# Kernel optimization log

Measured on AMD Instinct MI355X. Metric: run time of the kernel, lower is better.

The kernel has to match this reference:

```python
import jax, jax.numpy as jnp
import numpy as np
import math

DIM = 512
HEADS = 8
DIM_HEAD = 64
SCALE = math.sqrt(DIM_HEAD)
EPS = 1e-12


def rms_norm(x, g):
    # F.normalize(x, dim=1) * g * sqrt(dim); x: [B, C, H, W], g: [C]
    inv = jax.lax.rsqrt(jnp.sum(x * x, axis=1, keepdims=True) + EPS)
    return x * inv * g[None, :, None, None] * jnp.asarray(math.sqrt(x.shape[1]), x.dtype)


def setup_inputs() -> dict:
    key = jax.random.key(0)
    k1, k2, k3 = jax.random.split(key, 3)
    B, H, W = 8, 64, 64
    hidden = HEADS * DIM_HEAD
    x = jax.random.normal(k1, (B, DIM, H, W), dtype=jnp.float32)
    w_qkv = jax.random.normal(k2, (3 * hidden, DIM), dtype=jnp.float32) * (1.0 / math.sqrt(DIM))
    w_out = jax.random.normal(k3, (DIM, hidden), dtype=jnp.float32) * (1.0 / math.sqrt(hidden))
    b_out = jnp.zeros((DIM,), dtype=jnp.float32)
    g1 = jnp.ones((DIM,), dtype=jnp.float32)
    g2 = jnp.ones((DIM,), dtype=jnp.float32)
    return {"x": x, "g1": g1, "w_qkv": w_qkv, "w_out": w_out, "b_out": b_out, "g2": g2}


def reference(x, g1, w_qkv, w_out, b_out, g2):
    B, C, H, W = x.shape
    n = H * W
    xn = rms_norm(x, g1)
    # 1x1 conv == channel matmul: [B, 3*hidden, H, W]
    qkv = jnp.einsum('bchw,oc->bohw', xn, w_qkv)
    q, k, v = jnp.split(qkv, 3, axis=1)
    # b (h c) x y -> b h c n
    def to_heads(t):
        return t.reshape(B, HEADS, DIM_HEAD, n)
    q, k, v = to_heads(q), to_heads(k), to_heads(v)
    q = jax.nn.softmax(q, axis=2) / SCALE   # softmax over channel dim d
    k = jax.nn.softmax(k, axis=3)           # softmax over spatial dim n
    context = jnp.einsum('bhdn,bhen->bhde', k, v)   # [B, H, d, e]
    out = jnp.einsum('bhde,bhdn->bhen', context, q) # [B, H, e, n]
    out = out.reshape(B, HEADS * DIM_HEAD, H, W)
    out = jnp.einsum('bchw,oc->bohw', out, w_out) + b_out[None, :, None, None]
    return rms_norm(out, g2)
```

## Files before the change

kernel.cpp:

```cpp
#include <hip/hip_runtime.h>


typedef unsigned short u16;
typedef __attribute__((ext_vector_type(8))) short short8;
typedef __attribute__((ext_vector_type(4))) short short4_t;
typedef __attribute__((ext_vector_type(4))) float f32x4;

static constexpr size_t XN_B = (size_t)512 * 4096;
static constexpr size_t KV_B = (size_t)1024 * 4096;
static constexpr float SQRT512 = 22.62741699796952f;

typedef const __attribute__((address_space(1))) unsigned int gu32;
typedef __attribute__((address_space(3))) unsigned int lu32;

__device__ __forceinline__ float b2f(u16 u){
  union { unsigned u; float f; } x; x.u = ((unsigned)u) << 16; return x.f;
}
__device__ __forceinline__ u16 f2b(float f){
  union { float f; unsigned u; } x; x.f = f;
  unsigned r = x.u + 0x7FFFu + ((x.u >> 16) & 1u);
  return (u16)(r >> 16);
}
__device__ __forceinline__ void gl16(const u16* g, u16* l){
  __builtin_amdgcn_global_load_lds((gu32*)g, (lu32*)l, 16, 0, 0);
}

__global__ __launch_bounds__(256)
void kprep(const float* __restrict__ wqkv, const float* __restrict__ wout,
           const float* __restrict__ g1, u16* __restrict__ dq, u16* __restrict__ dw,
           const float* __restrict__ x, u16* __restrict__ xnT){
  __shared__ u16 lt[32][514];
  __shared__ float red[256];
  __shared__ float invs[32];
  int bid = blockIdx.x;
  int t = threadIdx.x;
  if (bid < 1024){
    size_t i = ((size_t)bid * 256 + t) * 4;
    short4_t o;
    if (i < (size_t)786432){
      f32x4 v = *(const f32x4*)(wqkv + i);
      int c = (int)(i & 511);
      #pragma unroll
      for (int j = 0; j < 4; j++) o[j] = (short)f2b(v[j] * g1[c + j] * SQRT512);
      *(short4_t*)(dq + i) = o;
    } else {
      size_t off = i - 786432;
      f32x4 v = *(const f32x4*)(wout + off);
      #pragma unroll
      for (int j = 0; j < 4; j++) o[j] = (short)f2b(v[j]);
      *(short4_t*)(dw + off) = o;
    }
    return;
  }
  int pg0 = (bid - 1024) * 32;
  int b = pg0 >> 12, p0 = pg0 & 4095;
  int px = t & 31, chunk = t >> 5;
  const float* xp = x + (size_t)b * XN_B + p0 + px;
  float s = 0.f;
  #pragma unroll 4
  for (int c = chunk * 64; c < chunk * 64 + 64; ++c){
    float v = xp[(size_t)c * 4096];
    lt[px][c] = f2b(v);
    s += v * v;
  }
  red[t] = s;
  __syncthreads();
  if (chunk == 0){
    float tt = red[px] + red[px + 32] + red[px + 64] + red[px + 96]
             + red[px + 128] + red[px + 160] + red[px + 192] + red[px + 224];
    invs[px] = rsqrtf(tt + 1e-12f);
  }
  __syncthreads();
  int px2 = t >> 3, c0 = (t & 7) * 8;
  float iv = invs[px2];
  u16* dst = xnT + (size_t)(pg0 + px2) * 512;
  #pragma unroll
  for (int j = 0; j < 8; j++){
    int c = c0 + j * 64;
    short8 o;
    #pragma unroll
    for (int e = 0; e < 8; e++) o[e] = (short)f2b(b2f(lt[px2][c + e]) * iv);
    *(short8*)(dst + c) = o;
  }
}

template<int ADD_BIAS, int SMAX>
__global__ __launch_bounds__(512)
void gemm_big(const u16* __restrict__ Ab, long astr, int lda,
              const u16* __restrict__ Bb, long bstr, int ldb,
              u16* __restrict__ Cb, long cstr, int ldc,
              const float* __restrict__ bias)
{
  constexpr int NT = 16;
  const u16* A  = Ab + (size_t)blockIdx.z * astr;
  const u16* BT = Bb + (size_t)blockIdx.z * bstr;
  u16* C = Cb + (size_t)blockIdx.z * cstr;
  const int m0 = blockIdx.y * 256, n0 = blockIdx.x * 256;
  __shared__ u16 As[2][256 * 32];
  __shared__ u16 Bs[2][256 * 32];
  const int tid = threadIdx.x;
  const int lane = tid & 63, wid = tid >> 6;
  const int wr = (wid >> 2) * 128, wc = (wid & 3) * 64;
  const int fr = lane & 15, fq = lane >> 4;
  const int srow = tid >> 2;
  const int sslot = tid & 3;
  f32x4 acc[8][4] = {};

  auto STAGE = [&](int s, int t){
    const int k0 = t * 32;
    #pragma unroll
    for (int r = 0; r < 2; r++){
      int row = r * 128 + srow;
      int gj = (sslot ^ ((row >> 1) & 3)) * 8;
      gl16(A  + (size_t)(m0 + row) * lda + k0 + gj, &As[s][0] + r * 4096 + tid * 8);
      gl16(BT + (size_t)(n0 + row) * ldb + k0 + gj, &Bs[s][0] + r * 4096 + tid * 8);
    }
  };

  STAGE(0, 0);
  int cur = 0;
  for (int t = 0; t < NT; t++){
    if (t + 1 < NT){
      STAGE(cur ^ 1, t + 1);
      asm volatile("s_waitcnt vmcnt(4)" ::: "memory");
    } else {
      asm volatile("s_waitcnt vmcnt(0)" ::: "memory");
    }
    __builtin_amdgcn_s_barrier();
    __builtin_amdgcn_sched_barrier(0);
    short8 a[8], b[4];
    #pragma unroll
    for (int i = 0; i < 8; i++){
      int ra = wr + i * 16 + fr;
      a[i] = *(const short8*)(&As[cur][0] + ra * 32 + ((fq ^ ((ra >> 1) & 3)) * 8));
    }
    #pragma unroll
    for (int j = 0; j < 4; j++){
      int rb = wc + j * 16 + fr;
      b[j] = *(const short8*)(&Bs[cur][0] + rb * 32 + ((fq ^ ((rb >> 1) & 3)) * 8));
    }
    __builtin_amdgcn_s_setprio(1);
    #pragma unroll
    for (int i = 0; i < 8; i++)
      #pragma unroll
      for (int j = 0; j < 4; j++)
        acc[i][j] = __builtin_amdgcn_mfma_f32_16x16x32_bf16(a[i], b[j], acc[i][j], 0, 0, 0);
    __builtin_amdgcn_s_setprio(0);
    __builtin_amdgcn_sched_barrier(0);
    __builtin_amdgcn_s_barrier();
    cur ^= 1;
  }

  if constexpr (SMAX){
    #pragma unroll
    for (int i = 0; i < 8; i++)
      #pragma unroll
      for (int e = 0; e < 4; e++){
        float mx = fmaxf(fmaxf(acc[i][0][e], acc[i][1][e]),
                         fmaxf(acc[i][2][e], acc[i][3][e]));
        mx = fmaxf(mx, __shfl_xor(mx, 1));
        mx = fmaxf(mx, __shfl_xor(mx, 2));
        mx = fmaxf(mx, __shfl_xor(mx, 4));
        mx = fmaxf(mx, __shfl_xor(mx, 8));
        float p0 = __expf(acc[i][0][e] - mx);
        float p1 = __expf(acc[i][1][e] - mx);
        float p2 = __expf(acc[i][2][e] - mx);
        float p3 = __expf(acc[i][3][e] - mx);
        float s = p0 + p1 + p2 + p3;
        s += __shfl_xor(s, 1);
        s += __shfl_xor(s, 2);
        s += __shfl_xor(s, 4);
        s += __shfl_xor(s, 8);
        float r = 1.f / (s * 8.0f);
        acc[i][0][e] = p0 * r; acc[i][1][e] = p1 * r;
        acc[i][2][e] = p2 * r; acc[i][3][e] = p3 * r;
      }
  }
  #pragma unroll
  for (int i = 0; i < 8; i++)
    #pragma unroll
    for (int j = 0; j < 4; j++)
      #pragma unroll
      for (int e = 0; e < 4; e++){
        int row = m0 + wr + i * 16 + fq * 4 + e;
        int col = n0 + wc + j * 16 + fr;
        float v = acc[i][j][e];
        if constexpr (ADD_BIAS) v += bias[col];
        C[(size_t)row * ldc + col] = f2b(v);
      }
}

__global__ __launch_bounds__(256)
void gemm_kv(const u16* __restrict__ Wkv, const u16* __restrict__ xnT,
             u16* __restrict__ kvb, float* __restrict__ stats)
{
  constexpr int NT = 8;
  const int z = blockIdx.z;
  const u16* A  = Wkv;
  const u16* BT = xnT + (size_t)z * XN_B;
  u16* C = kvb + (size_t)z * KV_B;
  const int m0 = blockIdx.y * 128, n0 = blockIdx.x * 128;
  __shared__ u16 As[2][128 * 64];
  __shared__ u16 Bs[2][128 * 64];
  const int tid = threadIdx.x;
  const int srow0 = tid >> 3;
  const int schunk = tid & 7;
  const int lane = tid & 63, wid = tid >> 6;
  const int wr = (wid >> 1) * 64, wc = (wid & 1) * 64;
  const int fr = lane & 15, fq = lane >> 4;
  f32x4 acc[4][4] = {};

  auto STAGE = [&](int s, int t){
    const int k0 = t * 64;
    #pragma unroll
    for (int r = 0; r < 4; r++){
      int row = r * 32 + srow0;
      int gj = (schunk ^ (row & 7)) * 8;
      gl16(A  + (size_t)(m0 + row) * 512 + k0 + gj, &As[s][0] + r * 2048 + tid * 8);
      gl16(BT + (size_t)(n0 + row) * 512 + k0 + gj, &Bs[s][0] + r * 2048 + tid * 8);
    }
  };

  STAGE(0, 0);
  int cur = 0;
  for (int t = 0; t < NT; t++){
    if (t + 1 < NT){
      STAGE(cur ^ 1, t + 1);
      asm volatile("s_waitcnt vmcnt(8)" ::: "memory");
    } else {
      asm volatile("s_waitcnt vmcnt(0)" ::: "memory");
    }
    __builtin_amdgcn_s_barrier();
    __builtin_amdgcn_sched_barrier(0);
    #pragma unroll
    for (int ks = 0; ks < 2; ks++){
      short8 a[4], b[4];
      #pragma unroll
      for (int i = 0; i < 4; i++){
        int ra = wr + i * 16 + fr;
        a[i] = *(const short8*)(&As[cur][0] + ra * 64 + ((ks * 4 + fq) ^ (ra & 7)) * 8);
        int rb = wc + i * 16 + fr;
        b[i] = *(const short8*)(&Bs[cur][0] + rb * 64 + ((ks * 4 + fq) ^ (rb & 7)) * 8);
      }
      __builtin_amdgcn_s_setprio(1);
      #pragma unroll
      for (int i = 0; i < 4; i++)
        #pragma unroll
        for (int j = 0; j < 4; j++)
          acc[i][j] = __builtin_amdgcn_mfma_f32_16x16x32_bf16(a[i], b[j], acc[i][j], 0, 0, 0);
      __builtin_amdgcn_s_setprio(0);
    }
    __builtin_amdgcn_sched_barrier(0);
    __builtin_amdgcn_s_barrier();
    cur ^= 1;
  }

  const bool krows = (m0 < 512);
  #pragma unroll
  for (int i = 0; i < 4; i++)
    #pragma unroll
    for (int e = 0; e < 4; e++){
      int row = m0 + wr + i * 16 + fq * 4 + e;
      float s = 0.f;
      #pragma unroll
      for (int j = 0; j < 4; j++){
        int col = n0 + wc + j * 16 + fr;
        u16 vc = f2b(acc[i][j][e]);
        C[(size_t)row * 4096 + col] = vc;
        if (krows) s += __expf(b2f(vc));
      }
      if (krows){
        s += __shfl_xor(s, 1);
        s += __shfl_xor(s, 2);
        s += __shfl_xor(s, 4);
        s += __shfl_xor(s, 8);
        if (fr == 0) atomicAdd(stats + z * 512 + row, s);
      }
    }
}

__global__ __launch_bounds__(256)
void gemm_ctx(const u16* __restrict__ kv, float* __restrict__ P,
              const float* __restrict__ stats)
{
  constexpr int K = 1024;
  const int z = blockIdx.z;
  const int tid = threadIdx.x;
  const int ar = tid >> 2, ac = (tid & 3) * 8;
  int bh = z >> 2, sp = z & 3, b = bh >> 3, h = bh & 7;
  const u16* A  = kv + (size_t)b * KV_B + (size_t)(h * 64) * 4096 + sp * 1024;
  const u16* BT = kv + (size_t)b * KV_B + (size_t)(512 + h * 64) * 4096 + sp * 1024;
  float rsr = 1.f / stats[b * 512 + h * 64 + ar];
  __shared__ u16 As[64 * 40];
  __shared__ u16 Bs[64 * 40];
  const int wid = tid >> 6, lane = tid & 63;
  const int wr = (wid >> 1) * 32, wc = (wid & 1) * 32;
  const int lr = lane & 15, kb = lane >> 4;
  f32x4 acc[2][2] = {};
  for (int k0 = 0; k0 < K; k0 += 32){
    short8 av = *(const short8*)(A + (size_t)ar * 4096 + k0 + ac);
    short8 ao;
    #pragma unroll
    for (int e = 0; e < 8; e++)
      ao[e] = (short)f2b(__expf(b2f((u16)av[e])) * rsr);
    *(short8*)(As + ar * 40 + ac) = ao;
    *(short8*)(Bs + ar * 40 + ac) = *(const short8*)(BT + (size_t)ar * 4096 + k0 + ac);
    __syncthreads();
    short8 a0 = *(const short8*)(As + (wr +      lr) * 40 + kb * 8);
    short8 a1 = *(const short8*)(As + (wr + 16 + lr) * 40 + kb * 8);
    short8 b0 = *(const short8*)(Bs + (wc +      lr) * 40 + kb * 8);
    short8 b1 = *(const short8*)(Bs + (wc + 16 + lr) * 40 + kb * 8);
    acc[0][0] = __builtin_amdgcn_mfma_f32_16x16x32_bf16(a0, b0, acc[0][0], 0, 0, 0);
    acc[0][1] = __builtin_amdgcn_mfma_f32_16x16x32_bf16(a0, b1, acc[0][1], 0, 0, 0);
    acc[1][0] = __builtin_amdgcn_mfma_f32_16x16x32_bf16(a1, b0, acc[1][0], 0, 0, 0);
    acc[1][1] = __builtin_amdgcn_mfma_f32_16x16x32_bf16(a1, b1, acc[1][1], 0, 0, 0);
    __syncthreads();
  }
  #pragma unroll
  for (int mi = 0; mi < 2; mi++)
    #pragma unroll
    for (int ni = 0; ni < 2; ni++)
      #pragma unroll
      for (int j = 0; j < 4; j++){
        int row = wr + mi * 16 + kb * 4 + j;
        int col = wc + ni * 16 + lr;
        P[(size_t)z * 4096 + (size_t)row * 64 + col] = acc[mi][ni][j];
      }
}

__global__ __launch_bounds__(256)
void kctxw(const float* __restrict__ P, const u16* __restrict__ woutbf,
           u16* __restrict__ M)
{
  const int z = blockIdx.z;
  const int b = z >> 3, h = z & 7;
  const int m0 = blockIdx.y * 64;
  const int tid = threadIdx.x;
  __shared__ u16 As[64 * 72];
  __shared__ u16 Bs[64 * 72];
  {
    int r = tid >> 2, c0 = (tid & 3) * 16;
    const u16* wsrc = woutbf + (size_t)(m0 + r) * 512 + h * 64 + c0;
    *(short8*)(As + r * 72 + c0)     = *(const short8*)(wsrc);
    *(short8*)(As + r * 72 + c0 + 8) = *(const short8*)(wsrc + 8);
    const float* p = P + (size_t)z * 16384 + (size_t)r * 64 + c0;
    #pragma unroll
    for (int e = 0; e < 16; e++){
      float s = p[e] + p[e + 4096] + p[e + 8192] + p[e + 12288];
      Bs[r * 72 + c0 + e] = f2b(s);
    }
  }
  __syncthreads();
  const int wid = tid >> 6, lane = tid & 63;
  const int wr = (wid >> 1) * 32, wc = (wid & 1) * 32;
  const int lr = lane & 15, kb = lane >> 4;
  f32x4 acc[2][2] = {};
  #pragma unroll
  for (int k0 = 0; k0 < 64; k0 += 32){
    short8 a0 = *(const short8*)(As + (wr +      lr) * 72 + k0 + kb * 8);
    short8 a1 = *(const short8*)(As + (wr + 16 + lr) * 72 + k0 + kb * 8);
    short8 b0 = *(const short8*)(Bs + (wc +      lr) * 72 + k0 + kb * 8);
    short8 b1 = *(const short8*)(Bs + (wc + 16 + lr) * 72 + k0 + kb * 8);
    acc[0][0] = __builtin_amdgcn_mfma_f32_16x16x32_bf16(a0, b0, acc[0][0], 0, 0, 0);
    acc[0][1] = __builtin_amdgcn_mfma_f32_16x16x32_bf16(a0, b1, acc[0][1], 0, 0, 0);
    acc[1][0] = __builtin_amdgcn_mfma_f32_16x16x32_bf16(a1, b0, acc[1][0], 0, 0, 0);
    acc[1][1] = __builtin_amdgcn_mfma_f32_16x16x32_bf16(a1, b1, acc[1][1], 0, 0, 0);
  }
  #pragma unroll
  for (int mi = 0; mi < 2; mi++)
    #pragma unroll
    for (int ni = 0; ni < 2; ni++)
      #pragma unroll
      for (int j = 0; j < 4; j++){
        int row = m0 + wr + mi * 16 + kb * 4 + j;
        int col = wc + ni * 16 + lr;
        M[(size_t)b * 262144 + (size_t)row * 512 + h * 64 + col] = f2b(acc[mi][ni][j]);
      }
}

__global__ __launch_bounds__(256)
void krms2(const u16* __restrict__ o2, const float* __restrict__ g,
           float* __restrict__ out){
  __shared__ u16 lt[32][514];
  __shared__ float invs[32];
  __shared__ float gl[512];
  int t = threadIdx.x;
  int pg0 = blockIdx.x * 32;
  int b = pg0 >> 12, p0 = pg0 & 4095;
  gl[t] = g[t] * SQRT512;
  gl[t + 256] = g[t + 256] * SQRT512;
  int px2 = t >> 3, c0 = (t & 7) * 8;
  const u16* src = o2 + (size_t)(pg0 + px2) * 512;
  float s = 0.f;
  #pragma unroll
  for (int j = 0; j < 8; j++){
    int c = c0 + j * 64;
    short8 v = *(const short8*)(src + c);
    *(short8*)&lt[px2][c] = v;
    #pragma unroll
    for (int e = 0; e < 8; e++){ float f = b2f((u16)v[e]); s += f * f; }
  }
  s += __shfl_xor(s, 1); s += __shfl_xor(s, 2); s += __shfl_xor(s, 4);
  if ((t & 7) == 0) invs[px2] = rsqrtf(s + 1e-12f);
  __syncthreads();
  int c2 = t >> 2, pxc = (t & 3) * 8;
  float ivv[8];
  #pragma unroll
  for (int e = 0; e < 8; e++) ivv[e] = invs[pxc + e];
  #pragma unroll
  for (int pass = 0; pass < 8; pass++){
    int c = c2 + pass * 64;
    float gf = gl[c];
    float* dst = out + ((size_t)(b * 512 + c)) * 4096 + p0 + pxc;
    #pragma unroll
    for (int q = 0; q < 2; q++){
      f32x4 o;
      #pragma unroll
      for (int e = 0; e < 4; e++){
        int pp = q * 4 + e;
        o[e] = b2f(lt[pxc + pp][c]) * ivv[pp] * gf;
      }
      *(f32x4*)(dst + q * 4) = o;
    }
  }
}

extern "C" void kernel_launch(void* const* d_in, const int* in_sizes, int n_in,
                              void* d_out, int out_size, void* d_ws, size_t ws_size,
                              hipStream_t stream)
{
  (void)in_sizes; (void)n_in; (void)out_size; (void)ws_size;
  const float* x    = (const float*)d_in[0];
  const float* g1   = (const float*)d_in[1];
  const float* wqkv = (const float*)d_in[2];
  const float* wout = (const float*)d_in[3];
  const float* bout = (const float*)d_in[4];
  const float* g2   = (const float*)d_in[5];
  float* out = (float*)d_out;
  char* ws = (char*)d_ws;

  u16*   xnT   = (u16*)(ws);
  float* P     = (float*)(ws);
  u16*   M     = (u16*)(ws + (size_t)8388608);
  u16*   qT    = (u16*)(ws + (size_t)33554432);
  u16*   kv    = (u16*)(ws + (size_t)67108864);
  u16*   out2T = (u16*)(ws + (size_t)67108864);
  u16*   wbf   = (u16*)(ws + (size_t)134217728);
  u16*   wkvbf = wbf + (size_t)512 * 512;
  u16*   woutbf= (u16*)(ws + (size_t)135790592);
  float* stats = (float*)(ws + (size_t)136314880);

  hipMemsetAsync(stats, 0, 4096 * sizeof(float), stream);
  kprep<<<2048, 256, 0, stream>>>(wqkv, wout, g1, wbf, woutbf, x, xnT);
  gemm_big<0, 1><<<dim3(2, 128, 1), 512, 0, stream>>>(xnT, 0, 512, wbf, 0, 512,
                                                      qT, 0, 512, nullptr);
  gemm_kv<<<dim3(32, 8, 8), 256, 0, stream>>>(wkvbf, xnT, kv, stats);
  gemm_ctx<<<dim3(1, 1, 256), 256, 0, stream>>>(kv, P, stats);
  kctxw<<<dim3(1, 8, 64), 256, 0, stream>>>(P, woutbf, M);
  gemm_big<1, 0><<<dim3(2, 16, 8), 512, 0, stream>>>(qT, (long)4096 * 512, 512,
                                                     M, (long)262144, 512,
                                                     out2T, (long)4096 * 512, 512, bout);
  krms2<<<1024, 256, 0, stream>>>(out2T, g2, out);
}
```

Before: 198.8 us.

## Move softmax row-sum stats to separate kernel and double ctx split-K

Removes the exp-sum and atomicAdd epilogue from the KV GEMM and computes the reciprocal row sums in a dedicated kstats kernel that rereads the K rows. The context GEMM now splits the spatial dimension 8 ways instead of 4, launching 512 blocks, and kctxw reduces 8 partials. It also drops the setprio hints and the stats memset. The intent is to shorten the GEMM epilogue, avoid contended atomics, and fill more CUs in the context step. The cost is an extra launch, an extra pass over the K half of kv, and a larger partial buffer to reduce.

```diff
diff --git a/kernel.cpp b/kernel.cpp
--- a/kernel.cpp
+++ b/kernel.cpp
@@ -192,7 +192,7 @@
 
 __global__ __launch_bounds__(256)
 void gemm_kv(const u16* __restrict__ Wkv, const u16* __restrict__ xnT,
-             u16* __restrict__ kvb, float* __restrict__ stats)
+             u16* __restrict__ kvb)
 {
   constexpr int NT = 8;
   const int z = blockIdx.z;
@@ -242,55 +242,63 @@
         int rb = wc + i * 16 + fr;
         b[i] = *(const short8*)(&Bs[cur][0] + rb * 64 + ((ks * 4 + fq) ^ (rb & 7)) * 8);
       }
-      __builtin_amdgcn_s_setprio(1);
       #pragma unroll
       for (int i = 0; i < 4; i++)
         #pragma unroll
         for (int j = 0; j < 4; j++)
           acc[i][j] = __builtin_amdgcn_mfma_f32_16x16x32_bf16(a[i], b[j], acc[i][j], 0, 0, 0);
-      __builtin_amdgcn_s_setprio(0);
     }
     __builtin_amdgcn_sched_barrier(0);
     __builtin_amdgcn_s_barrier();
     cur ^= 1;
   }
 
-  const bool krows = (m0 < 512);
   #pragma unroll
   for (int i = 0; i < 4; i++)
     #pragma unroll
-    for (int e = 0; e < 4; e++){
-      int row = m0 + wr + i * 16 + fq * 4 + e;
-      float s = 0.f;
-      #pragma unroll
-      for (int j = 0; j < 4; j++){
+    for (int j = 0; j < 4; j++)
+      #pragma unroll
+      for (int e = 0; e < 4; e++){
+        int row = m0 + wr + i * 16 + fq * 4 + e;
         int col = n0 + wc + j * 16 + fr;
-        u16 vc = f2b(acc[i][j][e]);
-        C[(size_t)row * 4096 + col] = vc;
-        if (krows) s += __expf(b2f(vc));
-      }
-      if (krows){
-        s += __shfl_xor(s, 1);
-        s += __shfl_xor(s, 2);
-        s += __shfl_xor(s, 4);
-        s += __shfl_xor(s, 8);
-        if (fr == 0) atomicAdd(stats + z * 512 + row, s);
-      }
-    }
+        C[(size_t)row * 4096 + col] = f2b(acc[i][j][e]);
+      }
+}
+
+__global__ __launch_bounds__(256)
+void kstats(const u16* __restrict__ kv, float* __restrict__ stats){
+  int bx = blockIdx.x;
+  int b = bx >> 9, c = bx & 511;
+  const u16* kp = kv + (size_t)b * KV_B + (size_t)c * 4096;
+  int tid = threadIdx.x;
+  float s = 0.f;
+  #pragma unroll
+  for (int j = 0; j < 2; j++){
+    short8 t = *(const short8*)(kp + j * 2048 + tid * 8);
+    #pragma unroll
+    for (int e = 0; e < 8; e++) s += __expf(b2f((u16)t[e]));
+  }
+  #pragma unroll
+  for (int o = 32; o >= 1; o >>= 1) s += __shfl_xor(s, o);
+  __shared__ float reds[4];
+  if ((tid & 63) == 0) reds[tid >> 6] = s;
+  __syncthreads();
+  if (tid == 0)
+    stats[bx] = 1.f / (reds[0] + reds[1] + reds[2] + reds[3]);
 }
 
 __global__ __launch_bounds__(256)
 void gemm_ctx(const u16* __restrict__ kv, float* __restrict__ P,
               const float* __restrict__ stats)
 {
-  constexpr int K = 1024;
+  constexpr int K = 512;
   const int z = blockIdx.z;
   const int tid = threadIdx.x;
   const int ar = tid >> 2, ac = (tid & 3) * 8;
-  int bh = z >> 2, sp = z & 3, b = bh >> 3, h = bh & 7;
-  const u16* A  = kv + (size_t)b * KV_B + (size_t)(h * 64) * 4096 + sp * 1024;
-  const u16* BT = kv + (size_t)b * KV_B + (size_t)(512 + h * 64) * 4096 + sp * 1024;
-  float rsr = 1.f / stats[b * 512 + h * 64 + ar];
+  int bh = z >> 3, sp = z & 7, b = bh >> 3, h = bh & 7;
+  const u16* A  = kv + (size_t)b * KV_B + (size_t)(h * 64) * 4096 + sp * 512;
+  const u16* BT = kv + (size_t)b * KV_B + (size_t)(512 + h * 64) * 4096 + sp * 512;
+  float rsr = stats[b * 512 + h * 64 + ar];
   __shared__ u16 As[64 * 40];
   __shared__ u16 Bs[64 * 40];
   const int wid = tid >> 6, lane = tid & 63;
@@ -343,10 +351,12 @@
     const u16* wsrc = woutbf + (size_t)(m0 + r) * 512 + h * 64 + c0;
     *(short8*)(As + r * 72 + c0)     = *(const short8*)(wsrc);
     *(short8*)(As + r * 72 + c0 + 8) = *(const short8*)(wsrc + 8);
-    const float* p = P + (size_t)z * 16384 + (size_t)r * 64 + c0;
+    const float* p = P + (size_t)z * 32768 + (size_t)r * 64 + c0;
     #pragma unroll
     for (int e = 0; e < 16; e++){
-      float s = p[e] + p[e + 4096] + p[e + 8192] + p[e + 12288];
+      float s = 0.f;
+      #pragma unroll
+      for (int sp = 0; sp < 8; sp++) s += p[e + sp * 4096];
       Bs[r * 72 + c0 + e] = f2b(s);
     }
   }
@@ -450,12 +460,12 @@
   u16*   woutbf= (u16*)(ws + (size_t)135790592);
   float* stats = (float*)(ws + (size_t)136314880);
 
-  hipMemsetAsync(stats, 0, 4096 * sizeof(float), stream);
   kprep<<<2048, 256, 0, stream>>>(wqkv, wout, g1, wbf, woutbf, x, xnT);
   gemm_big<0, 1><<<dim3(2, 128, 1), 512, 0, stream>>>(xnT, 0, 512, wbf, 0, 512,
                                                       qT, 0, 512, nullptr);
-  gemm_kv<<<dim3(32, 8, 8), 256, 0, stream>>>(wkvbf, xnT, kv, stats);
-  gemm_ctx<<<dim3(1, 1, 256), 256, 0, stream>>>(kv, P, stats);
+  gemm_kv<<<dim3(32, 8, 8), 256, 0, stream>>>(wkvbf, xnT, kv);
+  kstats<<<4096, 256, 0, stream>>>(kv, stats);
+  gemm_ctx<<<dim3(1, 1, 512), 256, 0, stream>>>(kv, P, stats);
   kctxw<<<dim3(1, 8, 64), 256, 0, stream>>>(P, woutbf, M);
   gemm_big<1, 0><<<dim3(2, 16, 8), 512, 0, stream>>>(qT, (long)4096 * 512, 512,
                                                      M, (long)262144, 512,
```

Result: faster. 191.0 us (-3.9%).

## Fuse K/V projection with context GEMM, dropping the K/V intermediate buffer

Applied to the files above, without the earlier changes.

The K/V projection kernel now tiles by head, loading the K and V weight rows for one head. It exponentiates the K tile and stages exp(K) and V in shared memory, then computes a partial k·vᵀ context per spatial tile and accumulates it into the global context with float atomics. This removes writing and re-reading the full bf16 K/V tensor and the separate context kernel. Softmax normalisation is deferred to kctxw, which divides by the accumulated denominators. The costs are many float atomics, with order-dependent rounding, and exp applied without max subtraction. s_setprio was also dropped.

```diff
diff --git a/kernel.cpp b/kernel.cpp
--- a/kernel.cpp
+++ b/kernel.cpp
@@ -7,7 +7,6 @@
 typedef __attribute__((ext_vector_type(4))) float f32x4;
 
 static constexpr size_t XN_B = (size_t)512 * 4096;
-static constexpr size_t KV_B = (size_t)1024 * 4096;
 static constexpr float SQRT512 = 22.62741699796952f;
 
 typedef const __attribute__((address_space(1))) unsigned int gu32;
@@ -191,15 +190,15 @@
 }
 
 __global__ __launch_bounds__(256)
-void gemm_kv(const u16* __restrict__ Wkv, const u16* __restrict__ xnT,
-             u16* __restrict__ kvb, float* __restrict__ stats)
+void gemm_kvctx(const u16* __restrict__ Wkv, const u16* __restrict__ xnT,
+                float* __restrict__ ctxE, float* __restrict__ sden)
 {
   constexpr int NT = 8;
   const int z = blockIdx.z;
-  const u16* A  = Wkv;
+  const int h = blockIdx.y;
+  const int bh = z * 8 + h;
   const u16* BT = xnT + (size_t)z * XN_B;
-  u16* C = kvb + (size_t)z * KV_B;
-  const int m0 = blockIdx.y * 128, n0 = blockIdx.x * 128;
+  const int n0 = blockIdx.x * 128;
   __shared__ u16 As[2][128 * 64];
   __shared__ u16 Bs[2][128 * 64];
   const int tid = threadIdx.x;
@@ -215,8 +214,9 @@
     #pragma unroll
     for (int r = 0; r < 4; r++){
       int row = r * 32 + srow0;
+      int grow = h * 64 + row + ((r >= 2) ? 448 : 0);
       int gj = (schunk ^ (row & 7)) * 8;
-      gl16(A  + (size_t)(m0 + row) * 512 + k0 + gj, &As[s][0] + r * 2048 + tid * 8);
+      gl16(Wkv + (size_t)grow * 512 + k0 + gj, &As[s][0] + r * 2048 + tid * 8);
       gl16(BT + (size_t)(n0 + row) * 512 + k0 + gj, &Bs[s][0] + r * 2048 + tid * 8);
     }
   };
@@ -242,95 +242,87 @@
         int rb = wc + i * 16 + fr;
         b[i] = *(const short8*)(&Bs[cur][0] + rb * 64 + ((ks * 4 + fq) ^ (rb & 7)) * 8);
       }
-      __builtin_amdgcn_s_setprio(1);
       #pragma unroll
       for (int i = 0; i < 4; i++)
         #pragma unroll
         for (int j = 0; j < 4; j++)
           acc[i][j] = __builtin_amdgcn_mfma_f32_16x16x32_bf16(a[i], b[j], acc[i][j], 0, 0, 0);
-      __builtin_amdgcn_s_setprio(0);
     }
     __builtin_amdgcn_sched_barrier(0);
     __builtin_amdgcn_s_barrier();
     cur ^= 1;
   }
 
-  const bool krows = (m0 < 512);
-  #pragma unroll
-  for (int i = 0; i < 4; i++)
-    #pragma unroll
-    for (int e = 0; e < 4; e++){
-      int row = m0 + wr + i * 16 + fq * 4 + e;
-      float s = 0.f;
-      #pragma unroll
-      for (int j = 0; j < 4; j++){
-        int col = n0 + wc + j * 16 + fr;
-        u16 vc = f2b(acc[i][j][e]);
-        C[(size_t)row * 4096 + col] = vc;
-        if (krows) s += __expf(b2f(vc));
-      }
-      if (krows){
+  u16* expK = &As[0][0];
+  u16* Vt   = &Bs[0][0];
+  if (wid < 2){
+    #pragma unroll
+    for (int i = 0; i < 4; i++)
+      #pragma unroll
+      for (int e = 0; e < 4; e++){
+        int row = i * 16 + fq * 4 + e;
+        float s = 0.f;
+        #pragma unroll
+        for (int j = 0; j < 4; j++){
+          int col = wc + j * 16 + fr;
+          u16 ub = f2b(__expf(acc[i][j][e]));
+          expK[row * 128 + (((col >> 3) ^ (row & 7)) << 3) + (col & 7)] = ub;
+          s += b2f(ub);
+        }
         s += __shfl_xor(s, 1);
         s += __shfl_xor(s, 2);
         s += __shfl_xor(s, 4);
         s += __shfl_xor(s, 8);
-        if (fr == 0) atomicAdd(stats + z * 512 + row, s);
-      }
-    }
+        if (fr == 0) atomicAdd(sden + bh * 64 + row, s);
+      }
+  } else {
+    #pragma unroll
+    for (int i = 0; i < 4; i++)
+      #pragma unroll
+      for (int e = 0; e < 4; e++){
+        int row = i * 16 + fq * 4 + e;
+        #pragma unroll
+        for (int j = 0; j < 4; j++){
+          int col = wc + j * 16 + fr;
+          Vt[row * 128 + (((col >> 3) ^ (row & 7)) << 3) + (col & 7)] = f2b(acc[i][j][e]);
+        }
+      }
+  }
+  __syncthreads();
+  const int er0 = (wid >> 1) * 32, ec0 = (wid & 1) * 32;
+  f32x4 acc2[2][2] = {};
+  #pragma unroll
+  for (int ks = 0; ks < 4; ks++){
+    short8 a2[2], b2[2];
+    #pragma unroll
+    for (int mi = 0; mi < 2; mi++){
+      int ra = er0 + mi * 16 + fr;
+      a2[mi] = *(const short8*)(expK + ra * 128 + (((ks * 4 + fq) ^ (ra & 7)) << 3));
+      int rb = ec0 + mi * 16 + fr;
+      b2[mi] = *(const short8*)(Vt + rb * 128 + (((ks * 4 + fq) ^ (rb & 7)) << 3));
+    }
+    #pragma unroll
+    for (int mi = 0; mi < 2; mi++)
+      #pragma unroll
+      for (int ni = 0; ni < 2; ni++)
+        acc2[mi][ni] = __builtin_amdgcn_mfma_f32_16x16x32_bf16(a2[mi], b2[ni], acc2[mi][ni], 0, 0, 0);
+  }
+  float* dst = ctxE + (size_t)bh * 4096;
+  #pragma unroll
+  for (int mi = 0; mi < 2; mi++)
+    #pragma unroll
+    for (int ni = 0; ni < 2; ni++)
+      #pragma unroll
+      for (int j = 0; j < 4; j++){
+        int d = er0 + mi * 16 + fq * 4 + j;
+        int e = ec0 + ni * 16 + fr;
+        atomicAdd(dst + d * 64 + e, acc2[mi][ni][j]);
+      }
 }
 
 __global__ __launch_bounds__(256)
-void gemm_ctx(const u16* __restrict__ kv, float* __restrict__ P,
-              const float* __restrict__ stats)
-{
-  constexpr int K = 1024;
-  const int z = blockIdx.z;
-  const int tid = threadIdx.x;
-  const int ar = tid >> 2, ac = (tid & 3) * 8;
-  int bh = z >> 2, sp = z & 3, b = bh >> 3, h = bh & 7;
-  const u16* A  = kv + (size_t)b * KV_B + (size_t)(h * 64) * 4096 + sp * 1024;
-  const u16* BT = kv + (size_t)b * KV_B + (size_t)(512 + h * 64) * 4096 + sp * 1024;
-  float rsr = 1.f / stats[b * 512 + h * 64 + ar];
-  __shared__ u16 As[64 * 40];
-  __shared__ u16 Bs[64 * 40];
-  const int wid = tid >> 6, lane = tid & 63;
-  const int wr = (wid >> 1) * 32, wc = (wid & 1) * 32;
-  const int lr = lane & 15, kb = lane >> 4;
-  f32x4 acc[2][2] = {};
-  for (int k0 = 0; k0 < K; k0 += 32){
-    short8 av = *(const short8*)(A + (size_t)ar * 4096 + k0 + ac);
-    short8 ao;
-    #pragma unroll
-    for (int e = 0; e < 8; e++)
-      ao[e] = (short)f2b(__expf(b2f((u16)av[e])) * rsr);
-    *(short8*)(As + ar * 40 + ac) = ao;
-    *(short8*)(Bs + ar * 40 + ac) = *(const short8*)(BT + (size_t)ar * 4096 + k0 + ac);
-    __syncthreads();
-    short8 a0 = *(const short8*)(As + (wr +      lr) * 40 + kb * 8);
-    short8 a1 = *(const short8*)(As + (wr + 16 + lr) * 40 + kb * 8);
-    short8 b0 = *(const short8*)(Bs + (wc +      lr) * 40 + kb * 8);
-    short8 b1 = *(const short8*)(Bs + (wc + 16 + lr) * 40 + kb * 8);
-    acc[0][0] = __builtin_amdgcn_mfma_f32_16x16x32_bf16(a0, b0, acc[0][0], 0, 0, 0);
-    acc[0][1] = __builtin_amdgcn_mfma_f32_16x16x32_bf16(a0, b1, acc[0][1], 0, 0, 0);
-    acc[1][0] = __builtin_amdgcn_mfma_f32_16x16x32_bf16(a1, b0, acc[1][0], 0, 0, 0);
-    acc[1][1] = __builtin_amdgcn_mfma_f32_16x16x32_bf16(a1, b1, acc[1][1], 0, 0, 0);
-    __syncthreads();
-  }
-  #pragma unroll
-  for (int mi = 0; mi < 2; mi++)
-    #pragma unroll
-    for (int ni = 0; ni < 2; ni++)
-      #pragma unroll
-      for (int j = 0; j < 4; j++){
-        int row = wr + mi * 16 + kb * 4 + j;
-        int col = wc + ni * 16 + lr;
-        P[(size_t)z * 4096 + (size_t)row * 64 + col] = acc[mi][ni][j];
-      }
-}
-
-__global__ __launch_bounds__(256)
-void kctxw(const float* __restrict__ P, const u16* __restrict__ woutbf,
-           u16* __restrict__ M)
+void kctxw(const float* __restrict__ ctxE, const float* __restrict__ sden,
+           const u16* __restrict__ woutbf, u16* __restrict__ M)
 {
   const int z = blockIdx.z;
   const int b = z >> 3, h = z & 7;
@@ -343,12 +335,11 @@
     const u16* wsrc = woutbf + (size_t)(m0 + r) * 512 + h * 64 + c0;
     *(short8*)(As + r * 72 + c0)     = *(const short8*)(wsrc);
     *(short8*)(As + r * 72 + c0 + 8) = *(const short8*)(wsrc + 8);
-    const float* p = P + (size_t)z * 16384 + (size_t)r * 64 + c0;
-    #pragma unroll
-    for (int e = 0; e < 16; e++){
-      float s = p[e] + p[e + 4096] + p[e + 8192] + p[e + 12288];
-      Bs[r * 72 + c0 + e] = f2b(s);
-    }
+    float rs = 1.f / sden[z * 64 + r];
+    const float* p = ctxE + (size_t)z * 4096 + (size_t)r * 64 + c0;
+    #pragma unroll
+    for (int e = 0; e < 16; e++)
+      Bs[r * 72 + c0 + e] = f2b(p[e] * rs);
   }
   __syncthreads();
   const int wid = tid >> 6, lane = tid & 63;
@@ -440,23 +431,21 @@
   char* ws = (char*)d_ws;
 
   u16*   xnT   = (u16*)(ws);
-  float* P     = (float*)(ws);
-  u16*   M     = (u16*)(ws + (size_t)8388608);
   u16*   qT    = (u16*)(ws + (size_t)33554432);
-  u16*   kv    = (u16*)(ws + (size_t)67108864);
+  float* ctxE  = (float*)(ws + (size_t)67108864);
+  float* sden  = (float*)(ws + (size_t)68157440);
   u16*   out2T = (u16*)(ws + (size_t)67108864);
+  u16*   M     = (u16*)(ws + (size_t)100663296);
   u16*   wbf   = (u16*)(ws + (size_t)134217728);
   u16*   wkvbf = wbf + (size_t)512 * 512;
   u16*   woutbf= (u16*)(ws + (size_t)135790592);
-  float* stats = (float*)(ws + (size_t)136314880);
-
-  hipMemsetAsync(stats, 0, 4096 * sizeof(float), stream);
+
+  hipMemsetAsync(ctxE, 0, (size_t)1048576 + 16384, stream);
   kprep<<<2048, 256, 0, stream>>>(wqkv, wout, g1, wbf, woutbf, x, xnT);
   gemm_big<0, 1><<<dim3(2, 128, 1), 512, 0, stream>>>(xnT, 0, 512, wbf, 0, 512,
                                                       qT, 0, 512, nullptr);
-  gemm_kv<<<dim3(32, 8, 8), 256, 0, stream>>>(wkvbf, xnT, kv, stats);
-  gemm_ctx<<<dim3(1, 1, 256), 256, 0, stream>>>(kv, P, stats);
-  kctxw<<<dim3(1, 8, 64), 256, 0, stream>>>(P, woutbf, M);
+  gemm_kvctx<<<dim3(32, 8, 8), 256, 0, stream>>>(wkvbf, xnT, ctxE, sden);
+  kctxw<<<dim3(1, 8, 64), 256, 0, stream>>>(ctxE, sden, woutbf, M);
   gemm_big<1, 0><<<dim3(2, 16, 8), 512, 0, stream>>>(qT, (long)4096 * 512, 512,
                                                      M, (long)262144, 512,
                                                      out2T, (long)4096 * 512, 512, bout);
```

New measurement: 192.2 us. -3.3%, faster.
